# Kernel optimization log

Hardware: AMD Instinct MI355X
Metric: run time of the kernel (lower is better)

The kernel has to match this reference:

```python
import jax, jax.numpy as jnp
import numpy as np

B, D, L = 32768, 1024, 4

def setup_inputs() -> dict:
    key = jax.random.key(0)
    k1, k2, k3 = jax.random.split(key, 3)
    x = jax.random.normal(k1, (B, D), dtype=jnp.float32)
    # torch init: normal_(0, 0.005) for both weights and biases, shape (d,1) -> flatten to (d,)
    weights = jax.random.normal(k2, (L, D), dtype=jnp.float32) * 0.005
    biases = jax.random.normal(k3, (L, D), dtype=jnp.float32) * 0.005
    return {"x": x, "weights": weights, "biases": biases}

def reference(x, weights, biases):
    # DCN cross layer: x_{i+1} = x0 * (x_i . w_i) + b_i + x_i
    # Algebraically identical to matmul(bmm(x0, x_i^T), w_i) + b_i + x_i
    x0 = x  # [B, D]

    def step(cur, wb):
        w, b = wb  # [D], [D]
        s = cur @ w  # [B] scalar per row (x_i^T w_i)
        cur = x0 * s[:, None] + b[None, :] + cur  # [B, D]
        return cur, None

    out, _ = jax.lax.scan(step, x, (weights, biases))
    return out  # [B, D] (squeeze of [B, D, 1])
```

## Files before the change

### kernel.cpp

```cpp
#include <hip/hip_runtime.h>


#define DCN_D 1024
#define DCN_L 4
#define DCN_BLOCK 256

__global__ __launch_bounds__(DCN_BLOCK) void dcn_cross_kernel(
    const float* __restrict__ x,
    const float* __restrict__ weights,
    const float* __restrict__ biases,
    float* __restrict__ out,
    int B)
{
    const int row = blockIdx.x;
    if (row >= B) return;
    const int t = threadIdx.x;

    const float4* __restrict__ xrow =
        reinterpret_cast<const float4*>(x + (size_t)row * DCN_D);
    const float4 x0 = xrow[t];
    float4 cur = x0;

    __shared__ float red[DCN_BLOCK / 64];

    const int wave = t >> 6;
    const int lane = t & 63;

    #pragma unroll
    for (int l = 0; l < DCN_L; ++l) {
        const float4 w =
            reinterpret_cast<const float4*>(weights + (size_t)l * DCN_D)[t];
        float p = cur.x * w.x;
        p = fmaf(cur.y, w.y, p);
        p = fmaf(cur.z, w.z, p);
        p = fmaf(cur.w, w.w, p);
        #pragma unroll
        for (int off = 32; off > 0; off >>= 1)
            p += __shfl_down(p, off, 64);
        if (lane == 0) red[wave] = p;
        __syncthreads();
        const float s = red[0] + red[1] + red[2] + red[3];

        const float4 b =
            reinterpret_cast<const float4*>(biases + (size_t)l * DCN_D)[t];
        cur.x = fmaf(x0.x, s, b.x + cur.x);
        cur.y = fmaf(x0.y, s, b.y + cur.y);
        cur.z = fmaf(x0.z, s, b.z + cur.z);
        cur.w = fmaf(x0.w, s, b.w + cur.w);
        __syncthreads();
    }

    reinterpret_cast<float4*>(out + (size_t)row * DCN_D)[t] = cur;
}

extern "C" void kernel_launch(void* const* d_in, const int* in_sizes, int n_in,
                              void* d_out, int out_size, void* d_ws, size_t ws_size,
                              hipStream_t stream) {
    const float* x = (const float*)d_in[0];
    const float* w = (const float*)d_in[1];
    const float* b = (const float*)d_in[2];
    float* out = (float*)d_out;
    const int B = in_sizes[0] / DCN_D;

    dcn_cross_kernel<<<B, DCN_BLOCK, 0, stream>>>(x, w, b, out, B);
}
```

Before: 60.84 us.

## Collapse four cross layers into one scalar per row via algebraic precompute

Uses the linearity of the recurrence, where each layer's output is x0 times an accumulated scalar plus a sum of biases, to rewrite the whole stack as out = x0*S + sum(b). A small pre-kernel computes the summed bias and the bias-weight dot products. The main kernel computes all four x0·w dot products in a single pass, with one wave per row, and reduces them with xor shuffles instead of shared memory and barriers. This removes the per-layer __syncthreads and serial reductions. It adds an extra tiny kernel launch and changes the floating-point summation order.

```diff
diff --git a/kernel.cpp b/kernel.cpp
--- a/kernel.cpp
+++ b/kernel.cpp
@@ -2,55 +2,105 @@
 
 
 #define DCN_D 1024
-#define DCN_L 4
-#define DCN_BLOCK 256
+#define DCN_F4 (DCN_D / 4)
 
-__global__ __launch_bounds__(DCN_BLOCK) void dcn_cross_kernel(
+
+__global__ __launch_bounds__(256) void dcn_pre_kernel(
+    const float* __restrict__ w,
+    const float* __restrict__ b,
+    float* __restrict__ ws)
+{
+    const int t = threadIdx.x;
+    for (int d = t; d < DCN_D; d += 256)
+        ws[d] = b[d] + b[DCN_D + d] + b[2 * DCN_D + d] + b[3 * DCN_D + d];
+    float p[6] = {0, 0, 0, 0, 0, 0};
+    for (int d = t; d < DCN_D; d += 256) {
+        const float b0 = b[d], b1 = b[DCN_D + d], b2 = b[2 * DCN_D + d];
+        const float w1 = w[DCN_D + d], w2 = w[2 * DCN_D + d], w3 = w[3 * DCN_D + d];
+        p[0] = fmaf(b0, w1, p[0]);
+        p[1] = fmaf(b0, w2, p[1]);
+        p[2] = fmaf(b1, w2, p[2]);
+        p[3] = fmaf(b0, w3, p[3]);
+        p[4] = fmaf(b1, w3, p[4]);
+        p[5] = fmaf(b2, w3, p[5]);
+    }
+    __shared__ float red[6][4];
+    const int wave = t >> 6, lane = t & 63;
+    #pragma unroll
+    for (int k = 0; k < 6; ++k) {
+        float v = p[k];
+        #pragma unroll
+        for (int off = 32; off > 0; off >>= 1) v += __shfl_down(v, off, 64);
+        if (lane == 0) red[k][wave] = v;
+    }
+    __syncthreads();
+    if (t < 6) ws[DCN_D + t] = red[t][0] + red[t][1] + red[t][2] + red[t][3];
+}
+
+__global__ __launch_bounds__(256) void dcn_main_kernel(
     const float* __restrict__ x,
-    const float* __restrict__ weights,
-    const float* __restrict__ biases,
+    const float* __restrict__ w,
+    const float* __restrict__ ws,
     float* __restrict__ out,
     int B)
 {
-    const int row = blockIdx.x;
+    const int row  = (int)((blockIdx.x * 256u + threadIdx.x) >> 6);
+    const int lane = threadIdx.x & 63;
     if (row >= B) return;
-    const int t = threadIdx.x;
 
-    const float4* __restrict__ xrow =
-        reinterpret_cast<const float4*>(x + (size_t)row * DCN_D);
-    const float4 x0 = xrow[t];
-    float4 cur = x0;
+    const float4* __restrict__ xr = reinterpret_cast<const float4*>(x + (size_t)row * DCN_D);
+    const float4* __restrict__ w4 = reinterpret_cast<const float4*>(w);
 
-    __shared__ float red[DCN_BLOCK / 64];
-
-    const int wave = t >> 6;
-    const int lane = t & 63;
+    float4 xv[4];
+    float p0 = 0.f, p1 = 0.f, p2 = 0.f, p3 = 0.f;
 
     #pragma unroll
-    for (int l = 0; l < DCN_L; ++l) {
-        const float4 w =
-            reinterpret_cast<const float4*>(weights + (size_t)l * DCN_D)[t];
-        float p = cur.x * w.x;
-        p = fmaf(cur.y, w.y, p);
-        p = fmaf(cur.z, w.z, p);
-        p = fmaf(cur.w, w.w, p);
-        #pragma unroll
-        for (int off = 32; off > 0; off >>= 1)
-            p += __shfl_down(p, off, 64);
-        if (lane == 0) red[wave] = p;
-        __syncthreads();
-        const float s = red[0] + red[1] + red[2] + red[3];
-
-        const float4 b =
-            reinterpret_cast<const float4*>(biases + (size_t)l * DCN_D)[t];
-        cur.x = fmaf(x0.x, s, b.x + cur.x);
-        cur.y = fmaf(x0.y, s, b.y + cur.y);
-        cur.z = fmaf(x0.z, s, b.z + cur.z);
-        cur.w = fmaf(x0.w, s, b.w + cur.w);
-        __syncthreads();
+    for (int j = 0; j < 4; ++j) {
+        const int idx = lane + 64 * j;
+        const float4 xc = xr[idx];
+        xv[j] = xc;
+        const float4 w0 = w4[idx];
+        const float4 w1 = w4[DCN_F4 + idx];
+        const float4 w2 = w4[2 * DCN_F4 + idx];
+        const float4 w3 = w4[3 * DCN_F4 + idx];
+        p0 = fmaf(xc.x, w0.x, fmaf(xc.y, w0.y, fmaf(xc.z, w0.z, fmaf(xc.w, w0.w, p0))));
+        p1 = fmaf(xc.x, w1.x, fmaf(xc.y, w1.y, fmaf(xc.z, w1.z, fmaf(xc.w, w1.w, p1))));
+        p2 = fmaf(xc.x, w2.x, fmaf(xc.y, w2.y, fmaf(xc.z, w2.z, fmaf(xc.w, w2.w, p2))));
+        p3 = fmaf(xc.x, w3.x, fmaf(xc.y, w3.y, fmaf(xc.z, w3.z, fmaf(xc.w, w3.w, p3))));
     }
 
-    reinterpret_cast<float4*>(out + (size_t)row * DCN_D)[t] = cur;
+    #pragma unroll
+    for (int off = 1; off < 64; off <<= 1) {
+        p0 += __shfl_xor(p0, off, 64);
+        p1 += __shfl_xor(p1, off, 64);
+        p2 += __shfl_xor(p2, off, 64);
+        p3 += __shfl_xor(p3, off, 64);
+    }
+
+    const float c01 = ws[DCN_D + 0], c02 = ws[DCN_D + 1], c12 = ws[DCN_D + 2];
+    const float c03 = ws[DCN_D + 3], c13 = ws[DCN_D + 4], c23 = ws[DCN_D + 5];
+    const float s0 = p0;
+    const float t1 = 1.f + s0;
+    const float s1 = fmaf(p1, t1, c01);
+    const float t2 = t1 + s1;
+    const float s2 = fmaf(p2, t2, c02 + c12);
+    const float t3 = t2 + s2;
+    const float s3 = fmaf(p3, t3, c03 + c13 + c23);
+    const float S  = t3 + s3;
+
+    const float4* __restrict__ bs4 = reinterpret_cast<const float4*>(ws);
+    float4* __restrict__ o4 = reinterpret_cast<float4*>(out + (size_t)row * DCN_D);
+    #pragma unroll
+    for (int j = 0; j < 4; ++j) {
+        const int idx = lane + 64 * j;
+        const float4 bb = bs4[idx];
+        float4 o;
+        o.x = fmaf(xv[j].x, S, bb.x);
+        o.y = fmaf(xv[j].y, S, bb.y);
+        o.z = fmaf(xv[j].z, S, bb.z);
+        o.w = fmaf(xv[j].w, S, bb.w);
+        o4[idx] = o;
+    }
 }
 
 extern "C" void kernel_launch(void* const* d_in, const int* in_sizes, int n_in,
@@ -60,7 +110,11 @@
     const float* w = (const float*)d_in[1];
     const float* b = (const float*)d_in[2];
     float* out = (float*)d_out;
+    float* ws = (float*)d_ws;
     const int B = in_sizes[0] / DCN_D;
 
-    dcn_cross_kernel<<<B, DCN_BLOCK, 0, stream>>>(x, w, b, out, B);
+    dcn_pre_kernel<<<1, 256, 0, stream>>>(w, b, ws);
+    const int rows_per_block = 4;
+    dcn_main_kernel<<<(B + rows_per_block - 1) / rows_per_block, 256, 0, stream>>>(
+        x, w, ws, out, B);
 }
```

New measurement: 51.38 us. 15.6% less time.
